# Kernel optimization log

Hardware: AMD Instinct MI355X
Metric: run time of the kernel (lower is better)

Reference implementation:

```python
import jax, jax.numpy as jnp
import numpy as np

B, T, H = 16, 2048, 768
HH = H // 2          # LSTM hidden per direction
L = 2                # interaction layers
NH = 8               # attention heads
SA, SO = 24, 24      # num aspect / opinion spans
WMAX = 16            # max span width (static)


def _make_spans(key, n_spans):
    # non-overlapping spans: one per chunk of size T//n_spans, width in [1, WMAX]
    chunk = T // n_spans
    k1, k2 = jax.random.split(key)
    off = jax.random.randint(k1, (B, n_spans), 0, chunk - WMAX)
    width = jax.random.randint(k2, (B, n_spans), 1, WMAX + 1)
    starts = jnp.arange(n_spans, dtype=jnp.int32)[None, :] * chunk + off
    return jnp.stack([starts, starts + width], axis=-1).astype(jnp.int32)


def setup_inputs() -> dict:
    key = jax.random.key(0)
    ks = jax.random.split(key, 20)
    p = lambda k, shape: jax.random.normal(k, shape, jnp.float32) * 0.02
    inp = {
        'hidden_states': jax.random.normal(ks[0], (B, T, H), jnp.float32),
        'aspect_spans': _make_spans(ks[1], SA),
        'opinion_spans': _make_spans(ks[2], SO),
    }
    # bidirectional LSTM span encoders (gate order i,f,g,o; bias = b_ih + b_hh)
    ki = 3
    for pre in ('a', 'o'):
        for d in ('f', 'b'):
            inp[f'{pre}_wih_{d}'] = p(ks[ki], (4 * HH, H)); ki += 1
            inp[f'{pre}_whh_{d}'] = p(ks[ki], (4 * HH, HH)); ki += 1
            inp[f'{pre}_b_{d}'] = jnp.zeros((4 * HH,), jnp.float32)
    # cross-attention stacks (torch nn.MultiheadAttention layout)
    for pre in ('ao', 'oa'):
        inp[f'attn_{pre}_in_w'] = p(ks[ki], (L, 3 * H, H)); ki += 1
        inp[f'attn_{pre}_in_b'] = jnp.zeros((L, 3 * H), jnp.float32)
        inp[f'attn_{pre}_out_w'] = p(ks[ki], (L, H, H)); ki += 1
        inp[f'attn_{pre}_out_b'] = jnp.zeros((L, H), jnp.float32)
    inp['ln_a_g'] = jnp.ones((L, H), jnp.float32)
    inp['ln_a_b'] = jnp.zeros((L, H), jnp.float32)
    inp['ln_o_g'] = jnp.ones((L, H), jnp.float32)
    inp['ln_o_b'] = jnp.zeros((L, H), jnp.float32)
    # span_interaction_projection: Linear(2H,H) -> ReLU -> Linear(H,H); stored [in,out]
    inp['p_w1'] = p(ks[ki], (2 * H, H)); ki += 1
    inp['p_b1'] = jnp.zeros((H,), jnp.float32)
    inp['p_w2'] = p(ks[ki], (H, H)); ki += 1
    inp['p_b2'] = jnp.zeros((H,), jnp.float32)
    return inp


def _lstm_span_encode(hs, spans, wih_f, whh_f, b_f, wih_b, whh_b, b_b):
    # batched replacement for the per-span python-loop LSTM calls
    Bn, Tn, Hd = hs.shape
    S = spans.shape[1]
    starts = jnp.clip(spans[..., 0], 0, Tn - 1)
    ends = jnp.clip(spans[..., 1], starts + 1, Tn)
    lens = (ends - starts).reshape(Bn * S)                              # [N]
    idx = jnp.clip(starts[..., None] + jnp.arange(WMAX), 0, Tn - 1)     # [B,S,W]
    x = hs[jnp.arange(Bn)[:, None, None], idx].reshape(Bn * S, WMAX, Hd)
    mask = jnp.arange(WMAX)[None, :] < lens[:, None]                    # [N,W]

    def step(carry, inp):
        h, c = carry
        x_t, m = inp
        g = x_t @ wih_f.T + h @ whh_f.T + b_f
        i, f, gg, o = jnp.split(g, 4, axis=-1)
        c_new = jax.nn.sigmoid(f) * c + jax.nn.sigmoid(i) * jnp.tanh(gg)
        h_new = jax.nn.sigmoid(o) * jnp.tanh(c_new)
        m = m[:, None]
        return (jnp.where(m, h_new, h), jnp.where(m, c_new, c)), None

    N = Bn * S
    h0 = jnp.zeros((N, HH), hs.dtype)
    (h_fwd, _), _ = jax.lax.scan(step, (h0, h0), (jnp.swapaxes(x, 0, 1), mask.T))
    # backward direction output at the original last step == one cell step from zero state
    x_last = jnp.take_along_axis(x, (lens - 1)[:, None, None], axis=1)[:, 0, :]
    g = x_last @ wih_b.T + b_b
    i, f, gg, o = jnp.split(g, 4, axis=-1)
    c_b = jax.nn.sigmoid(i) * jnp.tanh(gg)
    h_bwd = jax.nn.sigmoid(o) * jnp.tanh(c_b)
    return jnp.concatenate([h_fwd, h_bwd], -1).reshape(Bn, S, 2 * HH)


def _mha(q, kv, in_w, in_b, out_w, out_b):
    E = q.shape[-1]
    hd = E // NH
    wq, wk, wv = jnp.split(in_w, 3, axis=0)
    bq, bk, bv = jnp.split(in_b, 3, axis=0)
    qh = (q @ wq.T + bq).reshape(q.shape[0], q.shape[1], NH, hd)
    kh = (kv @ wk.T + bk).reshape(kv.shape[0], kv.shape[1], NH, hd)
    vh = (kv @ wv.T + bv).reshape(kv.shape[0], kv.shape[1], NH, hd)
    att = jax.nn.softmax(jnp.einsum('bqhd,bkhd->bhqk', qh, kh) * (1.0 / np.sqrt(hd)), axis=-1)
    out = jnp.einsum('bhqk,bkhd->bqhd', att, vh).reshape(q.shape)
    return out @ out_w.T + out_b


def _ln(x, g, b):
    mu = x.mean(-1, keepdims=True)
    var = ((x - mu) ** 2).mean(-1, keepdims=True)
    return (x - mu) * jax.lax.rsqrt(var + 1e-5) * g + b


def _apply_spans(tok, spans, reps, p_w1, p_b1, p_w2, p_b2):
    # vectorized version of the per-token projection loop (spans non-overlapping per set)
    Bn, Tn, Hd = tok.shape
    t = jnp.arange(Tn)
    starts = spans[..., 0]
    ends = jnp.minimum(spans[..., 1], Tn)
    cov = (t[None, :, None] >= starts[:, None, :]) & (t[None, :, None] < ends[:, None, :])  # [B,T,S]
    covered = cov.any(-1)
    sidx = jnp.argmax(cov, -1)                                   # [B,T]
    rep = reps[jnp.arange(Bn)[:, None], sidx]                    # [B,T,H]
    h1 = jax.nn.relu(jnp.concatenate([tok, rep], -1) @ p_w1 + p_b1)
    new = h1 @ p_w2 + p_b2
    return jnp.where(covered[..., None], new, tok)


def reference(hidden_states, a_wih_f, a_whh_f, a_b_f, a_wih_b, a_whh_b, a_b_b,
              o_wih_f, o_whh_f, o_b_f, o_wih_b, o_whh_b, o_b_b,
              attn_ao_in_w, attn_ao_in_b, attn_ao_out_w, attn_ao_out_b,
              attn_oa_in_w, attn_oa_in_b, attn_oa_out_w, attn_oa_out_b,
              ln_a_g, ln_a_b, ln_o_g, ln_o_b,
              p_w1, p_b1, p_w2, p_b2,
              aspect_spans, opinion_spans):
    ea = _lstm_span_encode(hidden_states, aspect_spans, a_wih_f, a_whh_f, a_b_f, a_wih_b, a_whh_b, a_b_b)
    eo = _lstm_span_encode(hidden_states, opinion_spans, o_wih_f, o_whh_f, o_b_f, o_wih_b, o_whh_b, o_b_b)
    for l in range(L):
        ea = _ln(ea + _mha(ea, eo, attn_ao_in_w[l], attn_ao_in_b[l], attn_ao_out_w[l], attn_ao_out_b[l]),
                 ln_a_g[l], ln_a_b[l])
        eo = _ln(eo + _mha(eo, ea, attn_oa_in_w[l], attn_oa_in_b[l], attn_oa_out_w[l], attn_oa_out_b[l]),
                 ln_o_g[l], ln_o_b[l])
    tok = _apply_spans(hidden_states, aspect_spans, ea, p_w1, p_b1, p_w2, p_b2)
    tok = _apply_spans(tok, opinion_spans, eo, p_w1, p_b1, p_w2, p_b2)
    return tok
```

## Files before the change

### kernel.cpp

```cpp
#include <hip/hip_runtime.h>
#include <cstddef>
#include <cstdint>

#define DI __device__ __forceinline__

namespace {

typedef short short8 __attribute__((ext_vector_type(8)));
typedef float f32x4 __attribute__((ext_vector_type(4)));

constexpr int B_ = 16, T_ = 2048, H_ = 768, HH_ = 384, NSPAN_ = 24;
constexpr int NS_ = B_ * NSPAN_;
constexpr int G4_ = 4 * HH_;
constexpr int WMAX_ = 16;
constexpr int MAXTOK_ = NS_ * WMAX_;

constexpr size_t W_AWIF = 0;
constexpr size_t W_OWIF = 1179648;
constexpr size_t W_AWIB = 2359296;
constexpr size_t W_OWIB = 3538944;
constexpr size_t W_AWHH = 4718592;
constexpr size_t W_OWHH = 5308416;
constexpr size_t W_AOIN = 5898240;
constexpr size_t W_OAIN = 9437184;
constexpr size_t W_AOOUT = 12976128;
constexpr size_t W_OAOUT = 14155776;
constexpr size_t W_PW1T = 15335424;
constexpr size_t W_PW2T = 16515072;
constexpr size_t W_TOTEL = 17104896;

constexpr size_t WB_B   = 0;
constexpr size_t WB_SZ  = W_TOTEL * 2;
constexpr size_t XGSZ_B = (size_t)NS_ * 16 * G4_ * 2;
constexpr size_t XGA_B  = WB_B + WB_SZ;
constexpr size_t XGO_B  = XGA_B + XGSZ_B;
constexpr size_t QKV_B  = XGO_B + XGSZ_B;
constexpr size_t AOT_B  = QKV_B + (size_t)NS_ * 2304 * 4;
constexpr size_t RT_B   = AOT_B + (size_t)NS_ * H_ * 4;
constexpr size_t EA_B   = RT_B + (size_t)NS_ * H_ * 4;
constexpr size_t EO_B   = EA_B + (size_t)NS_ * H_ * 4;
constexpr size_t HB_B   = EO_B + (size_t)NS_ * H_ * 4;
constexpr size_t CST_B  = HB_B + 2ull * 2 * 384 * 384 * 2;
constexpr size_t INT_B  = CST_B + 2ull * 384 * 384 * 4;
constexpr size_t I_STARTS = 0;
constexpr size_t I_LENS   = I_STARTS + 2 * NS_;
constexpr size_t I_ORD    = I_LENS + 2 * NS_;
constexpr size_t I_SLENS  = I_ORD + 2 * NS_;
constexpr size_t I_XGLIST = I_SLENS + 2 * NS_;
constexpr size_t I_TOKLIST = I_XGLIST + 2 * MAXTOK_;
constexpr size_t I_CNT    = I_TOKLIST + 2 * MAXTOK_;

DI float sigf(float x) { return 1.f / (1.f + __expf(-x)); }
DI float tanhfast(float x) {
  x = fminf(fmaxf(x, -15.f), 15.f);
  float e = __expf(2.f * x);
  return (e - 1.f) / (e + 1.f);
}
DI unsigned short f2bf(float f) {
  unsigned u = __float_as_uint(f);
  return (unsigned short)((u + 0x7fffu + ((u >> 16) & 1u)) >> 16);
}
DI unsigned pk2(float lo, float hi) {
  return (unsigned)f2bf(lo) | ((unsigned)f2bf(hi) << 16);
}
DI float bf2f(unsigned short u) { return __uint_as_float(((unsigned)u) << 16); }

struct PJ { const float* src; unsigned short* dst; int n; int R; int C; int tr; };
struct PREP { PJ j[12]; };

__global__ __launch_bounds__(256) void prep_w(PREP pp) {
  PJ job = pp.j[blockIdx.y];
  int stride = gridDim.x * blockDim.x;
  int g = blockIdx.x * blockDim.x + threadIdx.x;
  if (!job.tr) {
    int n4 = job.n >> 2;
    for (int i = g; i < n4; i += stride) {
      float4 v = ((const float4*)job.src)[i];
      ushort4 o;
      o.x = f2bf(v.x); o.y = f2bf(v.y); o.z = f2bf(v.z); o.w = f2bf(v.w);
      ((ushort4*)job.dst)[i] = o;
    }
  } else {
    for (int i = g; i < job.n; i += stride) {
      int r = i / job.C, c = i - r * job.C;
      job.dst[(size_t)c * job.R + r] = f2bf(job.src[i]);
    }
  }
}

__global__ void span_meta(const int* __restrict__ asp, const int* __restrict__ osp,
                          int* __restrict__ starts, int* __restrict__ lens,
                          int* __restrict__ xglist, int* __restrict__ cnt) {
  int i = blockIdx.x * blockDim.x + threadIdx.x;
  if (i >= 2 * NS_) return;
  int type = i / NS_, sp = i - type * NS_;
  const int* spans = type ? osp : asp;
  int s0 = spans[2 * sp], s1 = spans[2 * sp + 1];
  int st = min(max(s0, 0), T_ - 1);
  int en = min(max(s1, st + 1), T_);
  int ln = min(en - st, WMAX_);
  starts[i] = st;
  lens[i] = ln;
  for (int t = 0; t < ln; ++t) {
    int pos = atomicAdd(&cnt[type], 1);
    if (pos < MAXTOK_) xglist[type * MAXTOK_ + pos] = (sp << 4) | t;
  }
}

__global__ void sort_spans(const int* __restrict__ lens, int* __restrict__ ord,
                           int* __restrict__ slens) {
  int type = blockIdx.x;
  __shared__ int ls[NS_];
  __shared__ int os[NS_];
  __shared__ int hist[WMAX_], off[WMAX_];
  int tid = threadIdx.x;
  if (tid < WMAX_) hist[tid] = 0;
  __syncthreads();
  int myl = 1;
  if (tid < NS_) {
    myl = lens[type * NS_ + tid];
    ls[tid] = myl;
    atomicAdd(&hist[WMAX_ - myl], 1);
  }
  __syncthreads();
  if (tid == 0) { int a = 0; for (int b = 0; b < WMAX_; ++b) { off[b] = a; a += hist[b]; } }
  __syncthreads();
  if (tid < NS_) { int pos = atomicAdd(&off[WMAX_ - myl], 1); os[pos] = tid; }
  __syncthreads();
  if (tid < NS_) { int sp = os[tid]; ord[type * NS_ + tid] = sp; slens[type * NS_ + tid] = ls[sp]; }
}

__global__ void cov_build(const int* __restrict__ asp, const int* __restrict__ osp,
                          int* __restrict__ toklist, int* __restrict__ cnt2) {
  int i = blockIdx.x * blockDim.x + threadIdx.x;
  if (i >= 2 * NS_) return;
  int type = i / NS_, sp = i - type * NS_;
  const int* spans = type ? osp : asp;
  int b = sp / NSPAN_, s = sp - b * NSPAN_;
  int s0 = spans[2 * sp];
  int s1 = min(spans[2 * sp + 1], T_);
  int lo = max(s0, 0), hi = min(s1, s0 + WMAX_);
  for (int tt = lo; tt < hi; ++tt) {
    int pos = atomicAdd(&cnt2[type], 1);
    if (pos < MAXTOK_) toklist[type * MAXTOK_ + pos] = (b * T_ + tt) | (s << 20);
  }
}

enum { M_XG = 0, M_XGB = 1, M_QKV = 2, M_OUTP = 3, M_AP1 = 4, M_AP2 = 5 };

struct GP {
  const float* A;
  const float* A2;
  const unsigned short* Wb;
  const unsigned short* Ab;
  const float* bias;
  const float* resid;
  float* C;
  unsigned short* Cb;
  const int* list;
  const int* cnt;
  const int* starts;
  const int* lens;
  int K;
};

template <int MODE>
__global__ __launch_bounds__(256) void mgemm(GP p) {
  __shared__ __align__(16) unsigned short As[128 * 64];
  __shared__ __align__(16) unsigned short Bs[128 * 64];
  const int tid = threadIdx.x;
  const int m0 = blockIdx.x * 128, n0 = blockIdx.y * 128;
  int rows = NS_;
  if constexpr (MODE == M_XG || MODE == M_AP1 || MODE == M_AP2) rows = min(*p.cnt, MAXTOK_);
  if (m0 >= rows) return;

  const int ar = tid >> 1, kh = tid & 1;
  const int lr = m0 + ar;
  const bool aok = lr < rows;
  const float* aptr = nullptr;
  const float* aptr2 = nullptr;
  const unsigned short* abptr = nullptr;
  if (aok) {
    if constexpr (MODE == M_XG) {
      int e = p.list[lr]; int sp = e >> 4, tt = e & 15;
      int srow = min(p.starts[sp] + tt, T_ - 1);
      aptr = p.A + ((size_t)((sp / NSPAN_) * T_ + srow)) * H_;
    } else if constexpr (MODE == M_XGB) {
      int sp = lr;
      int srow = min(max(p.starts[sp] + p.lens[sp] - 1, 0), T_ - 1);
      aptr = p.A + ((size_t)((sp / NSPAN_) * T_ + srow)) * H_;
    } else if constexpr (MODE == M_QKV) {
      aptr = ((n0 < H_) ? p.A : p.A2) + (size_t)lr * H_;
    } else if constexpr (MODE == M_OUTP) {
      aptr = p.A + (size_t)lr * H_;
    } else if constexpr (MODE == M_AP1) {
      int e = p.list[lr]; int bt = e & 0xFFFFF; int s = e >> 20;
      aptr = p.A + (size_t)bt * H_;
      aptr2 = p.A2 + ((size_t)((bt >> 11) * NSPAN_ + s)) * H_;
    } else {
      abptr = p.Ab + (size_t)lr * H_;
    }
  }
  const unsigned short* brow = p.Wb + (size_t)(n0 + ar) * p.K;

  const int lane = tid & 63, wv = tid >> 6, wr = wv >> 1, wc = wv & 1;
  const int abase_r = wr * 64 + (lane & 15);
  const int bbase_r = wc * 64 + (lane & 15);
  const int kcol = lane >> 4;
  const int swz = (lane & 7) << 4;

  f32x4 acc[4][4];
#pragma unroll
  for (int mi = 0; mi < 4; ++mi)
#pragma unroll
    for (int ni = 0; ni < 4; ++ni) acc[mi][ni] = (f32x4){0.f, 0.f, 0.f, 0.f};

  for (int k0 = 0; k0 < p.K; k0 += 64) {
    if constexpr (MODE == M_AP2) {
      if (aok) {
        const unsigned short* s = abptr + k0 + kh * 32;
#pragma unroll
        for (int c = 0; c < 4; ++c)
          *(uint4*)((char*)As + ar * 128 + ((((kh * 4 + c) * 16)) ^ ((ar & 7) << 4))) =
              *(const uint4*)(s + c * 8);
      }
    } else {
      if (aok) {
#pragma unroll
        for (int c = 0; c < 4; ++c) {
          int kg = k0 + kh * 32 + c * 8;
          const float* s;
          if constexpr (MODE == M_AP1) s = (kg < H_) ? (aptr + kg) : (aptr2 + (kg - H_));
          else s = aptr + kg;
          float4 u = *(const float4*)s;
          float4 v = *(const float4*)(s + 4);
          uint4 w;
          w.x = pk2(u.x, u.y); w.y = pk2(u.z, u.w);
          w.z = pk2(v.x, v.y); w.w = pk2(v.z, v.w);
          *(uint4*)((char*)As + ar * 128 + ((((kh * 4 + c) * 16)) ^ ((ar & 7) << 4))) = w;
        }
      }
    }
    {
      const unsigned short* s = brow + k0 + kh * 32;
#pragma unroll
      for (int c = 0; c < 4; ++c)
        *(uint4*)((char*)Bs + ar * 128 + ((((kh * 4 + c) * 16)) ^ ((ar & 7) << 4))) =
            *(const uint4*)(s + c * 8);
    }
    __syncthreads();
#pragma unroll
    for (int ks = 0; ks < 2; ++ks) {
      short8 af[4], bq[4];
#pragma unroll
      for (int i = 0; i < 4; ++i)
        af[i] = *(const short8*)((char*)As + (abase_r + i * 16) * 128 +
                                 (((ks * 4 + kcol) * 16) ^ swz));
#pragma unroll
      for (int i = 0; i < 4; ++i)
        bq[i] = *(const short8*)((char*)Bs + (bbase_r + i * 16) * 128 +
                                 (((ks * 4 + kcol) * 16) ^ swz));
#pragma unroll
      for (int mi = 0; mi < 4; ++mi)
#pragma unroll
        for (int ni = 0; ni < 4; ++ni)
          acc[mi][ni] = __builtin_amdgcn_mfma_f32_16x16x32_bf16(af[mi], bq[ni], acc[mi][ni], 0, 0, 0);
    }
    __syncthreads();
  }

#pragma unroll
  for (int mi = 0; mi < 4; ++mi) {
#pragma unroll
    for (int q = 0; q < 4; ++q) {
      int row = m0 + wr * 64 + mi * 16 + (lane >> 4) * 4 + q;
      if (row >= rows) continue;
      if constexpr (MODE == M_XG) {
        int e = p.list[row]; int sp = e >> 4, tt = e & 15;
        unsigned short* cr = p.Cb + ((size_t)(sp * 16 + tt)) * G4_;
#pragma unroll
        for (int ni = 0; ni < 4; ++ni) {
          int col = n0 + wc * 64 + ni * 16 + (lane & 15);
          cr[col] = f2bf(acc[mi][ni][q] + p.bias[col]);
        }
      } else if constexpr (MODE == M_XGB) {
        float* cr = p.C + (size_t)row * G4_;
#pragma unroll
        for (int ni = 0; ni < 4; ++ni) {
          int col = n0 + wc * 64 + ni * 16 + (lane & 15);
          cr[col] = acc[mi][ni][q] + p.bias[col];
        }
      } else if constexpr (MODE == M_QKV) {
        float* cr = p.C + (size_t)row * 2304;
#pragma unroll
        for (int ni = 0; ni < 4; ++ni) {
          int col = n0 + wc * 64 + ni * 16 + (lane & 15);
          cr[col] = acc[mi][ni][q] + p.bias[col];
        }
      } else if constexpr (MODE == M_OUTP) {
        float* cr = p.C + (size_t)row * H_;
#pragma unroll
        for (int ni = 0; ni < 4; ++ni) {
          int col = n0 + wc * 64 + ni * 16 + (lane & 15);
          cr[col] = acc[mi][ni][q] + p.bias[col] + p.resid[(size_t)row * H_ + col];
        }
      } else if constexpr (MODE == M_AP1) {
        unsigned short* cr = p.Cb + (size_t)row * H_;
#pragma unroll
        for (int ni = 0; ni < 4; ++ni) {
          int col = n0 + wc * 64 + ni * 16 + (lane & 15);
          cr[col] = f2bf(fmaxf(acc[mi][ni][q] + p.bias[col], 0.f));
        }
      } else {
        int e = p.list[row]; int bt = e & 0xFFFFF;
        float* cr = p.C + (size_t)bt * H_;
#pragma unroll
        for (int ni = 0; ni < 4; ++ni) {
          int col = n0 + wc * 64 + ni * 16 + (lane & 15);
          cr[col] = acc[mi][ni][q] + p.bias[col];
        }
      }
    }
  }
}

__global__ void bwd_act(const float* __restrict__ gb, float* __restrict__ ea,
                        float* __restrict__ eo) {
  int idx = blockIdx.x * 256 + threadIdx.x;
  if (idx >= 2 * NS_ * HH_) return;
  int type = idx / (NS_ * HH_);
  int rem = idx - type * NS_ * HH_;
  int sp = rem / HH_, j = rem - sp * HH_;
  const float* g = gb + ((size_t)type * NS_ + sp) * G4_;
  float cb = sigf(g[j]) * tanhfast(g[2 * HH_ + j]);
  float hb = sigf(g[3 * HH_ + j]) * tanhfast(cb);
  (type ? eo : ea)[(size_t)sp * H_ + HH_ + j] = hb;
}

struct LP {
  const unsigned short* hr;
  unsigned short* hw;
  float* c;
  const unsigned short* xg_a;
  const unsigned short* xg_o;
  const unsigned short* whh_a;
  const unsigned short* whh_o;
  const int* ord; const int* slens;
  int t;
};

__global__ __launch_bounds__(256) void lstm_mfma(LP p) {
  const int type = blockIdx.z;
  const int m0 = blockIdx.x * 128;
  const int jb = blockIdx.y * 32;
  const int tid = threadIdx.x;
  const unsigned short* hr = p.hr + (size_t)type * 384 * 384;
  unsigned short* hw = p.hw + (size_t)type * 384 * 384;
  const int* slens = p.slens + type * NS_;

  if (slens[m0] <= p.t) {
    int r = tid >> 1, ch = tid & 1;
    const unsigned short* s = hr + (size_t)(m0 + r) * 384 + jb + ch * 16;
    unsigned short* d = hw + (size_t)(m0 + r) * 384 + jb + ch * 16;
    *(uint4*)d = *(const uint4*)s;
    *(uint4*)(d + 8) = *(const uint4*)(s + 8);
    return;
  }

  const unsigned short* xg = type ? p.xg_o : p.xg_a;
  const unsigned short* whh = type ? p.whh_o : p.whh_a;
  const int* ordt = p.ord + type * NS_;
  float* cst = p.c + (size_t)type * 384 * 384;

  __shared__ __align__(16) unsigned short As[128 * 64];
  __shared__ __align__(16) unsigned short Bs[128 * 64];

  const int ar = tid >> 1, kh = tid & 1;
  const unsigned short* arow = hr + (size_t)(m0 + ar) * 384;
  const int ng = ((ar >> 4) & 3) * HH_ + jb + (ar >> 6) * 16 + (ar & 15);
  const unsigned short* brow = whh + (size_t)ng * HH_;

  const int lane = tid & 63, wv = tid >> 6, wr = wv >> 1, wc = wv & 1;
  const int abase_r = wr * 64 + (lane & 15);
  const int bbase_r = wc * 64 + (lane & 15);
  const int kcol = lane >> 4;
  const int swz = (lane & 7) << 4;

  f32x4 acc[4][4];
#pragma unroll
  for (int mi = 0; mi < 4; ++mi)
#pragma unroll
    for (int ni = 0; ni < 4; ++ni) acc[mi][ni] = (f32x4){0.f, 0.f, 0.f, 0.f};

  for (int k0 = 0; k0 < HH_; k0 += 64) {
    const unsigned short* sa = arow + k0 + kh * 32;
    const unsigned short* sb = brow + k0 + kh * 32;
#pragma unroll
    for (int c = 0; c < 4; ++c) {
      *(uint4*)((char*)As + ar * 128 + ((((kh * 4 + c) * 16)) ^ ((ar & 7) << 4))) =
          *(const uint4*)(sa + c * 8);
      *(uint4*)((char*)Bs + ar * 128 + ((((kh * 4 + c) * 16)) ^ ((ar & 7) << 4))) =
          *(const uint4*)(sb + c * 8);
    }
    __syncthreads();
#pragma unroll
    for (int ks = 0; ks < 2; ++ks) {
      short8 af[4], bq[4];
#pragma unroll
      for (int i = 0; i < 4; ++i)
        af[i] = *(const short8*)((char*)As + (abase_r + i * 16) * 128 +
                                 (((ks * 4 + kcol) * 16) ^ swz));
#pragma unroll
      for (int i = 0; i < 4; ++i)
        bq[i] = *(const short8*)((char*)Bs + (bbase_r + i * 16) * 128 +
                                 (((ks * 4 + kcol) * 16) ^ swz));
#pragma unroll
      for (int mi = 0; mi < 4; ++mi)
#pragma unroll
        for (int ni = 0; ni < 4; ++ni)
          acc[mi][ni] = __builtin_amdgcn_mfma_f32_16x16x32_bf16(af[mi], bq[ni], acc[mi][ni], 0, 0, 0);
    }
    __syncthreads();
  }

  const int col = jb + wc * 16 + (lane & 15);
#pragma unroll
  for (int mi = 0; mi < 4; ++mi) {
#pragma unroll
    for (int q = 0; q < 4; ++q) {
      int row = m0 + wr * 64 + mi * 16 + (lane >> 4) * 4 + q;
      int sp = ordt[row];
      bool act = p.t < slens[row];
      const unsigned short* xr = xg + ((size_t)(sp * 16 + p.t)) * G4_;
      float gi = acc[mi][0][q] + bf2f(xr[col]);
      float gf = acc[mi][1][q] + bf2f(xr[HH_ + col]);
      float gg = acc[mi][2][q] + bf2f(xr[2 * HH_ + col]);
      float go = acc[mi][3][q] + bf2f(xr[3 * HH_ + col]);
      size_t hidx = (size_t)row * 384 + col;
      unsigned short hraw = hr[hidx];
      float co = cst[hidx];
      float cn = sigf(gf) * co + sigf(gi) * tanhfast(gg);
      float hn = sigf(go) * tanhfast(cn);
      hw[hidx] = act ? f2bf(hn) : hraw;
      if (act) cst[hidx] = cn;
    }
  }
}

__global__ void finalize_h(const unsigned short* __restrict__ hfin,
                           const int* __restrict__ ord,
                           float* __restrict__ ea, float* __restrict__ eo) {
  int idx = blockIdx.x * 256 + threadIdx.x;
  if (idx >= 2 * 384 * 384) return;
  int type = idx / (384 * 384);
  int rem = idx - type * 384 * 384;
  int srt = rem / 384, j = rem - srt * 384;
  int sp = ord[type * NS_ + srt];
  (type ? eo : ea)[(size_t)sp * H_ + j] =
      bf2f(hfin[(size_t)type * 384 * 384 + (size_t)srt * 384 + j]);
}

__global__ __launch_bounds__(256) void attn_core(const float* __restrict__ qkv,
                                                 float* __restrict__ aot) {
  int b = blockIdx.x >> 3, h = blockIdx.x & 7;
  __shared__ float qs[24][97], ks[24][97], vs[24][97];
  __shared__ float sc[24][25];
  __shared__ float sinv[24];
  int tid = threadIdx.x;
  for (int idx = tid; idx < 24 * 96; idx += 256) {
    int s = idx / 96, d = idx - s * 96;
    size_t rb = ((size_t)(b * 24 + s)) * 2304 + h * 96 + d;
    qs[s][d] = qkv[rb];
    ks[s][d] = qkv[rb + H_];
    vs[s][d] = qkv[rb + 2 * H_];
  }
  __syncthreads();
  for (int pp = tid; pp < 576; pp += 256) {
    int qi = pp / 24, ki = pp - qi * 24;
    float a = 0.f;
    for (int d = 0; d < 96; ++d) a = fmaf(qs[qi][d], ks[ki][d], a);
    sc[qi][ki] = a * 0.10206207261596577f;
  }
  __syncthreads();
  if (tid < 24) {
    float m = -1e30f;
    for (int k2 = 0; k2 < 24; ++k2) m = fmaxf(m, sc[tid][k2]);
    float ssum = 0.f;
    for (int k2 = 0; k2 < 24; ++k2) { float e = __expf(sc[tid][k2] - m); sc[tid][k2] = e; ssum += e; }
    sinv[tid] = 1.f / ssum;
  }
  __syncthreads();
  for (int idx = tid; idx < 24 * 96; idx += 256) {
    int s = idx / 96, d = idx - s * 96;
    float a = 0.f;
    for (int k2 = 0; k2 < 24; ++k2) a = fmaf(sc[s][k2], vs[k2][d], a);
    aot[((size_t)(b * 24 + s)) * H_ + h * 96 + d] = a * sinv[s];
  }
}

__global__ __launch_bounds__(256) void ln_k(const float* __restrict__ x,
                                            const float* __restrict__ g,
                                            const float* __restrict__ bb,
                                            float* __restrict__ dst) {
  int row = blockIdx.x;
  const float* xr = x + (size_t)row * H_;
  float vals[3];
  float s1 = 0.f, s2 = 0.f;
#pragma unroll
  for (int u = 0; u < 3; ++u) {
    float v = xr[threadIdx.x + 256 * u];
    vals[u] = v; s1 += v; s2 += v * v;
  }
  for (int o = 32; o > 0; o >>= 1) { s1 += __shfl_down(s1, o, 64); s2 += __shfl_down(s2, o, 64); }
  __shared__ float r1[4], r2[4];
  __shared__ float mu_s, rs_s;
  int w = threadIdx.x >> 6, lane = threadIdx.x & 63;
  if (lane == 0) { r1[w] = s1; r2[w] = s2; }
  __syncthreads();
  if (threadIdx.x == 0) {
    float t1 = r1[0] + r1[1] + r1[2] + r1[3];
    float t2 = r2[0] + r2[1] + r2[2] + r2[3];
    float mu = t1 / (float)H_;
    float var = t2 / (float)H_ - mu * mu;
    mu_s = mu; rs_s = rsqrtf(var + 1e-5f);
  }
  __syncthreads();
#pragma unroll
  for (int u = 0; u < 3; ++u) {
    int c = threadIdx.x + 256 * u;
    dst[(size_t)row * H_ + c] = (vals[u] - mu_s) * rs_s * g[c] + bb[c];
  }
}

}

extern "C" void kernel_launch(void* const* d_in, const int* in_sizes, int n_in,
                              void* d_out, int out_size, void* d_ws, size_t ws_size,
                              hipStream_t stream) {
  (void)in_sizes; (void)n_in; (void)out_size; (void)ws_size;
  const float* hs = (const float*)d_in[0];
  const int* asp = (const int*)d_in[1];
  const int* osp = (const int*)d_in[2];
  const float* a_wih_f = (const float*)d_in[3];
  const float* a_whh_f = (const float*)d_in[4];
  const float* a_b_f   = (const float*)d_in[5];
  const float* a_wih_b = (const float*)d_in[6];
  const float* a_b_b   = (const float*)d_in[8];
  const float* o_wih_f = (const float*)d_in[9];
  const float* o_whh_f = (const float*)d_in[10];
  const float* o_b_f   = (const float*)d_in[11];
  const float* o_wih_b = (const float*)d_in[12];
  const float* o_b_b   = (const float*)d_in[14];
  const float* ao_in_w  = (const float*)d_in[15];
  const float* ao_in_b  = (const float*)d_in[16];
  const float* ao_out_w = (const float*)d_in[17];
  const float* ao_out_b = (const float*)d_in[18];
  const float* oa_in_w  = (const float*)d_in[19];
  const float* oa_in_b  = (const float*)d_in[20];
  const float* oa_out_w = (const float*)d_in[21];
  const float* oa_out_b = (const float*)d_in[22];
  const float* ln_a_g = (const float*)d_in[23];
  const float* ln_a_b = (const float*)d_in[24];
  const float* ln_o_g = (const float*)d_in[25];
  const float* ln_o_b = (const float*)d_in[26];
  const float* p_w1 = (const float*)d_in[27];
  const float* p_b1 = (const float*)d_in[28];
  const float* p_w2 = (const float*)d_in[29];
  const float* p_b2 = (const float*)d_in[30];
  float* out = (float*)d_out;

  char* ws = (char*)d_ws;
  unsigned short* WB = (unsigned short*)(ws + WB_B);
  unsigned short* xga = (unsigned short*)(ws + XGA_B);
  unsigned short* xgo = (unsigned short*)(ws + XGO_B);
  float* qkv = (float*)(ws + QKV_B);
  float* aot = (float*)(ws + AOT_B);
  float* rt  = (float*)(ws + RT_B);
  float* ea  = (float*)(ws + EA_B);
  float* eo  = (float*)(ws + EO_B);
  unsigned short* hb = (unsigned short*)(ws + HB_B);
  float* cst = (float*)(ws + CST_B);
  float* gb  = (float*)(ws + QKV_B);
  unsigned short* h1b = (unsigned short*)(ws + XGA_B);
  int* I = (int*)(ws + INT_B);
  int* starts = I + I_STARTS;
  int* lens   = I + I_LENS;
  int* ord    = I + I_ORD;
  int* slens  = I + I_SLENS;
  int* xglist = I + I_XGLIST;
  int* toklist = I + I_TOKLIST;
  int* cnt    = I + I_CNT;

  hipMemcpyAsync(out, hs, (size_t)B_ * T_ * H_ * sizeof(float),
                 hipMemcpyDeviceToDevice, stream);
  hipMemsetAsync(cnt, 0, 4 * sizeof(int), stream);
  hipMemsetAsync(ws + HB_B, 0, (CST_B - HB_B) + 2ull * 384 * 384 * 4, stream);

  {
    PREP pp;
    pp.j[0]  = {a_wih_f,  WB + W_AWIF,  1536 * 768, 0, 0, 0};
    pp.j[1]  = {o_wih_f,  WB + W_OWIF,  1536 * 768, 0, 0, 0};
    pp.j[2]  = {a_wih_b,  WB + W_AWIB,  1536 * 768, 0, 0, 0};
    pp.j[3]  = {o_wih_b,  WB + W_OWIB,  1536 * 768, 0, 0, 0};
    pp.j[4]  = {a_whh_f,  WB + W_AWHH,  1536 * 384, 0, 0, 0};
    pp.j[5]  = {o_whh_f,  WB + W_OWHH,  1536 * 384, 0, 0, 0};
    pp.j[6]  = {ao_in_w,  WB + W_AOIN,  2 * 2304 * 768, 0, 0, 0};
    pp.j[7]  = {oa_in_w,  WB + W_OAIN,  2 * 2304 * 768, 0, 0, 0};
    pp.j[8]  = {ao_out_w, WB + W_AOOUT, 2 * 768 * 768, 0, 0, 0};
    pp.j[9]  = {oa_out_w, WB + W_OAOUT, 2 * 768 * 768, 0, 0, 0};
    pp.j[10] = {p_w1,     WB + W_PW1T,  1536 * 768, 1536, 768, 1};
    pp.j[11] = {p_w2,     WB + W_PW2T,  768 * 768,  768,  768, 1};
    prep_w<<<dim3(512, 12), 256, 0, stream>>>(pp);
  }

  span_meta<<<3, 256, 0, stream>>>(asp, osp, starts, lens, xglist, cnt);
  sort_spans<<<2, 384, 0, stream>>>(lens, ord, slens);
  cov_build<<<3, 256, 0, stream>>>(asp, osp, toklist, cnt + 2);

  {
    GP g{}; g.A = hs; g.Wb = WB + W_AWIF; g.bias = a_b_f; g.Cb = xga;
    g.list = xglist; g.cnt = cnt; g.starts = starts; g.K = H_;
    mgemm<M_XG><<<dim3(48, 12), 256, 0, stream>>>(g);
  }
  {
    GP g{}; g.A = hs; g.Wb = WB + W_OWIF; g.bias = o_b_f; g.Cb = xgo;
    g.list = xglist + MAXTOK_; g.cnt = cnt + 1; g.starts = starts + NS_; g.K = H_;
    mgemm<M_XG><<<dim3(48, 12), 256, 0, stream>>>(g);
  }
  {
    GP g{}; g.A = hs; g.Wb = WB + W_AWIB; g.bias = a_b_b; g.C = gb;
    g.starts = starts; g.lens = lens; g.K = H_;
    mgemm<M_XGB><<<dim3(3, 12), 256, 0, stream>>>(g);
  }
  {
    GP g{}; g.A = hs; g.Wb = WB + W_OWIB; g.bias = o_b_b; g.C = gb + (size_t)NS_ * G4_;
    g.starts = starts + NS_; g.lens = lens + NS_; g.K = H_;
    mgemm<M_XGB><<<dim3(3, 12), 256, 0, stream>>>(g);
  }
  bwd_act<<<(2 * NS_ * HH_ + 255) / 256, 256, 0, stream>>>(gb, ea, eo);

  for (int t = 0; t < 16; ++t) {
    LP lp{};
    lp.hr = hb + (size_t)(t & 1) * 2 * 384 * 384;
    lp.hw = hb + (size_t)((t + 1) & 1) * 2 * 384 * 384;
    lp.c = cst;
    lp.xg_a = xga; lp.xg_o = xgo;
    lp.whh_a = WB + W_AWHH; lp.whh_o = WB + W_OWHH;
    lp.ord = ord; lp.slens = slens; lp.t = t;
    lstm_mfma<<<dim3(3, 12, 2), 256, 0, stream>>>(lp);
  }
  finalize_h<<<(2 * 384 * 384 + 255) / 256, 256, 0, stream>>>(hb, ord, ea, eo);

  for (int l = 0; l < 2; ++l) {
    for (int dir = 0; dir < 2; ++dir) {
      float* q  = dir ? eo : ea;
      float* kv = dir ? ea : eo;
      const unsigned short* inw = WB + (dir ? W_OAIN : W_AOIN) + (size_t)l * 2304 * 768;
      const float* inb = (dir ? oa_in_b : ao_in_b) + (size_t)l * 3 * H_;
      const unsigned short* ow = WB + (dir ? W_OAOUT : W_AOOUT) + (size_t)l * 768 * 768;
      const float* ob = (dir ? oa_out_b : ao_out_b) + (size_t)l * H_;
      const float* lg = (dir ? ln_o_g : ln_a_g) + (size_t)l * H_;
      const float* lb = (dir ? ln_o_b : ln_a_b) + (size_t)l * H_;
      {
        GP g{}; g.A = q; g.A2 = kv; g.Wb = inw; g.bias = inb; g.C = qkv; g.K = H_;
        mgemm<M_QKV><<<dim3(3, 18), 256, 0, stream>>>(g);
      }
      attn_core<<<128, 256, 0, stream>>>(qkv, aot);
      {
        GP g{}; g.A = aot; g.Wb = ow; g.bias = ob; g.resid = q; g.C = rt; g.K = H_;
        mgemm<M_OUTP><<<dim3(3, 6), 256, 0, stream>>>(g);
      }
      ln_k<<<NS_, 256, 0, stream>>>(rt, lg, lb, q);
    }
  }

  for (int type = 0; type < 2; ++type) {
    {
      GP g{}; g.A = out; g.A2 = type ? eo : ea; g.Wb = WB + W_PW1T; g.bias = p_b1; g.Cb = h1b;
      g.list = toklist + (size_t)type * MAXTOK_; g.cnt = cnt + 2 + type; g.K = 2 * H_;
      mgemm<M_AP1><<<dim3(48, 6), 256, 0, stream>>>(g);
    }
    {
      GP g{}; g.Ab = h1b; g.Wb = WB + W_PW2T; g.bias = p_b2; g.C = out;
      g.list = toklist + (size_t)type * MAXTOK_; g.cnt = cnt + 2 + type; g.K = H_;
      mgemm<M_AP2><<<dim3(48, 6), 256, 0, stream>>>(g);
    }
  }
}
```

Before: 1.519 ms.

## Fuse span metadata kernels, fuse backward LSTM gates, tile weight transpose

Merges span_meta, sort_spans and cov_build into one block-wide scan kernel, which replaces global atomics with deterministic prefix sums and drops the counter memset. Fuses the backward-direction input GEMMs for both span types with the gate activation into a single MFMA kernel whose weight rows are permuted so the i/g/o gates land in the same lanes, removing the intermediate gate buffer. The transposing weight conversion now goes through a shared-memory tile so global accesses are coalesced. The LSTM step also skips the h-buffer copy when a span finished more than one step earlier, relying on double-buffer parity.

```diff
diff --git a/kernel.cpp b/kernel.cpp
--- a/kernel.cpp
+++ b/kernel.cpp
@@ -70,9 +70,9 @@
 
 __global__ __launch_bounds__(256) void prep_w(PREP pp) {
   PJ job = pp.j[blockIdx.y];
-  int stride = gridDim.x * blockDim.x;
-  int g = blockIdx.x * blockDim.x + threadIdx.x;
   if (!job.tr) {
+    int stride = gridDim.x * blockDim.x;
+    int g = blockIdx.x * blockDim.x + threadIdx.x;
     int n4 = job.n >> 2;
     for (int i = g; i < n4; i += stride) {
       float4 v = ((const float4*)job.src)[i];
@@ -81,72 +81,99 @@
       ((ushort4*)job.dst)[i] = o;
     }
   } else {
-    for (int i = g; i < job.n; i += stride) {
-      int r = i / job.C, c = i - r * job.C;
-      job.dst[(size_t)c * job.R + r] = f2bf(job.src[i]);
-    }
-  }
-}
-
-__global__ void span_meta(const int* __restrict__ asp, const int* __restrict__ osp,
-                          int* __restrict__ starts, int* __restrict__ lens,
-                          int* __restrict__ xglist, int* __restrict__ cnt) {
-  int i = blockIdx.x * blockDim.x + threadIdx.x;
-  if (i >= 2 * NS_) return;
-  int type = i / NS_, sp = i - type * NS_;
+    __shared__ unsigned short tile[32][34];
+    int R = job.R, C = job.C;
+    int tcn = C >> 5, trn = R >> 5;
+    int tx = threadIdx.x & 31, ty = threadIdx.x >> 5;
+    for (int tid2 = blockIdx.x; tid2 < trn * tcn; tid2 += gridDim.x) {
+      int trr = (tid2 / tcn) << 5, tcc = (tid2 % tcn) << 5;
+      __syncthreads();
+#pragma unroll
+      for (int k = 0; k < 4; ++k)
+        tile[ty + 8 * k][tx] = f2bf(job.src[(size_t)(trr + ty + 8 * k) * C + tcc + tx]);
+      __syncthreads();
+#pragma unroll
+      for (int k = 0; k < 4; ++k)
+        job.dst[(size_t)(tcc + ty + 8 * k) * R + trr + tx] = tile[tx][ty + 8 * k];
+    }
+  }
+}
+
+__global__ __launch_bounds__(768) void span_prep(
+    const int* __restrict__ asp, const int* __restrict__ osp,
+    int* __restrict__ starts, int* __restrict__ lens,
+    int* __restrict__ ord, int* __restrict__ slens,
+    int* __restrict__ xglist, int* __restrict__ toklist, int* __restrict__ cnt) {
+  int tid = threadIdx.x;
+  int type = tid / NS_, sp = tid - type * NS_;
   const int* spans = type ? osp : asp;
   int s0 = spans[2 * sp], s1 = spans[2 * sp + 1];
   int st = min(max(s0, 0), T_ - 1);
   int en = min(max(s1, st + 1), T_);
   int ln = min(en - st, WMAX_);
-  starts[i] = st;
-  lens[i] = ln;
-  for (int t = 0; t < ln; ++t) {
-    int pos = atomicAdd(&cnt[type], 1);
-    if (pos < MAXTOK_) xglist[type * MAXTOK_ + pos] = (sp << 4) | t;
-  }
-}
-
-__global__ void sort_spans(const int* __restrict__ lens, int* __restrict__ ord,
-                           int* __restrict__ slens) {
-  int type = blockIdx.x;
-  __shared__ int ls[NS_];
-  __shared__ int os[NS_];
-  __shared__ int hist[WMAX_], off[WMAX_];
-  int tid = threadIdx.x;
-  if (tid < WMAX_) hist[tid] = 0;
-  __syncthreads();
-  int myl = 1;
-  if (tid < NS_) {
-    myl = lens[type * NS_ + tid];
-    ls[tid] = myl;
-    atomicAdd(&hist[WMAX_ - myl], 1);
-  }
-  __syncthreads();
-  if (tid == 0) { int a = 0; for (int b = 0; b < WMAX_; ++b) { off[b] = a; a += hist[b]; } }
-  __syncthreads();
-  if (tid < NS_) { int pos = atomicAdd(&off[WMAX_ - myl], 1); os[pos] = tid; }
-  __syncthreads();
-  if (tid < NS_) { int sp = os[tid]; ord[type * NS_ + tid] = sp; slens[type * NS_ + tid] = ls[sp]; }
-}
-
-__global__ void cov_build(const int* __restrict__ asp, const int* __restrict__ osp,
-                          int* __restrict__ toklist, int* __restrict__ cnt2) {
-  int i = blockIdx.x * blockDim.x + threadIdx.x;
-  if (i >= 2 * NS_) return;
-  int type = i / NS_, sp = i - type * NS_;
-  const int* spans = type ? osp : asp;
-  int b = sp / NSPAN_, s = sp - b * NSPAN_;
-  int s0 = spans[2 * sp];
-  int s1 = min(spans[2 * sp + 1], T_);
-  int lo = max(s0, 0), hi = min(s1, s0 + WMAX_);
-  for (int tt = lo; tt < hi; ++tt) {
-    int pos = atomicAdd(&cnt2[type], 1);
-    if (pos < MAXTOK_) toklist[type * MAXTOK_ + pos] = (b * T_ + tt) | (s << 20);
-  }
-}
-
-enum { M_XG = 0, M_XGB = 1, M_QKV = 2, M_OUTP = 3, M_AP1 = 4, M_AP2 = 5 };
+  starts[tid] = st;
+  lens[tid] = ln;
+  int clo = max(s0, 0), chi = min(s1, T_);
+  int cln = max(chi - clo, 0);
+
+  __shared__ int sx[768];
+  __shared__ int t0s, t0c;
+  sx[tid] = ln;
+  __syncthreads();
+  for (int off = 1; off < 768; off <<= 1) {
+    int v = (tid >= off) ? sx[tid - off] : 0;
+    __syncthreads();
+    sx[tid] += v;
+    __syncthreads();
+  }
+  if (tid == NS_ - 1) t0s = sx[tid];
+  __syncthreads();
+  {
+    int base = sx[tid] - ln - (type ? t0s : 0);
+    for (int t = 0; t < ln; ++t) {
+      int pos = base + t;
+      if (pos < MAXTOK_) xglist[type * MAXTOK_ + pos] = (sp << 4) | t;
+    }
+    if (tid == NS_ - 1) cnt[0] = sx[tid];
+    if (tid == 767) cnt[1] = sx[767] - t0s;
+  }
+  __syncthreads();
+  sx[tid] = cln;
+  __syncthreads();
+  for (int off = 1; off < 768; off <<= 1) {
+    int v = (tid >= off) ? sx[tid - off] : 0;
+    __syncthreads();
+    sx[tid] += v;
+    __syncthreads();
+  }
+  if (tid == NS_ - 1) t0c = sx[tid];
+  __syncthreads();
+  {
+    int base = sx[tid] - cln - (type ? t0c : 0);
+    int b = sp / NSPAN_, slocal = sp - b * NSPAN_;
+    for (int t = 0; t < cln; ++t) {
+      int pos = base + t;
+      if (pos < MAXTOK_) toklist[type * MAXTOK_ + pos] = (b * T_ + clo + t) | (slocal << 20);
+    }
+    if (tid == NS_ - 1) cnt[2] = sx[tid];
+    if (tid == 767) cnt[3] = sx[767] - t0c;
+  }
+  __shared__ int hist[2][WMAX_], hoff[2][WMAX_];
+  if (tid < 2 * WMAX_) hist[tid / WMAX_][tid % WMAX_] = 0;
+  __syncthreads();
+  atomicAdd(&hist[type][WMAX_ - ln], 1);
+  __syncthreads();
+  if (tid < 2) {
+    int a = 0;
+    for (int bkt = 0; bkt < WMAX_; ++bkt) { hoff[tid][bkt] = a; a += hist[tid][bkt]; }
+  }
+  __syncthreads();
+  int pos = atomicAdd(&hoff[type][WMAX_ - ln], 1);
+  ord[type * NS_ + pos] = sp;
+  slens[type * NS_ + pos] = ln;
+}
+
+enum { M_XG = 0, M_QKV = 2, M_OUTP = 3, M_AP1 = 4, M_AP2 = 5 };
 
 struct GP {
   const float* A;
@@ -160,7 +187,6 @@
   const int* list;
   const int* cnt;
   const int* starts;
-  const int* lens;
   int K;
 };
 
@@ -184,10 +210,6 @@
     if constexpr (MODE == M_XG) {
       int e = p.list[lr]; int sp = e >> 4, tt = e & 15;
       int srow = min(p.starts[sp] + tt, T_ - 1);
-      aptr = p.A + ((size_t)((sp / NSPAN_) * T_ + srow)) * H_;
-    } else if constexpr (MODE == M_XGB) {
-      int sp = lr;
-      int srow = min(max(p.starts[sp] + p.lens[sp] - 1, 0), T_ - 1);
       aptr = p.A + ((size_t)((sp / NSPAN_) * T_ + srow)) * H_;
     } else if constexpr (MODE == M_QKV) {
       aptr = ((n0 < H_) ? p.A : p.A2) + (size_t)lr * H_;
@@ -283,13 +305,6 @@
           int col = n0 + wc * 64 + ni * 16 + (lane & 15);
           cr[col] = f2bf(acc[mi][ni][q] + p.bias[col]);
         }
-      } else if constexpr (MODE == M_XGB) {
-        float* cr = p.C + (size_t)row * G4_;
-#pragma unroll
-        for (int ni = 0; ni < 4; ++ni) {
-          int col = n0 + wc * 64 + ni * 16 + (lane & 15);
-          cr[col] = acc[mi][ni][q] + p.bias[col];
-        }
       } else if constexpr (MODE == M_QKV) {
         float* cr = p.C + (size_t)row * 2304;
 #pragma unroll
@@ -324,17 +339,94 @@
   }
 }
 
-__global__ void bwd_act(const float* __restrict__ gb, float* __restrict__ ea,
-                        float* __restrict__ eo) {
-  int idx = blockIdx.x * 256 + threadIdx.x;
-  if (idx >= 2 * NS_ * HH_) return;
-  int type = idx / (NS_ * HH_);
-  int rem = idx - type * NS_ * HH_;
-  int sp = rem / HH_, j = rem - sp * HH_;
-  const float* g = gb + ((size_t)type * NS_ + sp) * G4_;
-  float cb = sigf(g[j]) * tanhfast(g[2 * HH_ + j]);
-  float hb = sigf(g[3 * HH_ + j]) * tanhfast(cb);
-  (type ? eo : ea)[(size_t)sp * H_ + HH_ + j] = hb;
+struct XBP {
+  const float* hs;
+  const unsigned short* wa; const unsigned short* wo;
+  const float* ba; const float* bo;
+  float* ea; float* eo;
+  const int* starts; const int* lens;
+};
+
+__global__ __launch_bounds__(256) void xgb_mfma(XBP p) {
+  const int type = blockIdx.z;
+  const int m0 = blockIdx.x * 128, jb = blockIdx.y * 32;
+  const int tid = threadIdx.x;
+  const unsigned short* wb = type ? p.wo : p.wa;
+  const float* bias = type ? p.bo : p.ba;
+  const int* starts = p.starts + type * NS_;
+  const int* lens = p.lens + type * NS_;
+  float* dst = type ? p.eo : p.ea;
+
+  __shared__ __align__(16) unsigned short As[128 * 64];
+  __shared__ __align__(16) unsigned short Bs[128 * 64];
+
+  const int ar = tid >> 1, kh = tid & 1;
+  const int spA = m0 + ar;
+  int srow = min(max(starts[spA] + lens[spA] - 1, 0), T_ - 1);
+  const float* aptr = p.hs + ((size_t)((spA / NSPAN_) * T_ + srow)) * H_;
+  const int ng = ((ar >> 4) & 3) * HH_ + jb + (ar >> 6) * 16 + (ar & 15);
+  const unsigned short* brow = wb + (size_t)ng * H_;
+
+  const int lane = tid & 63, wv = tid >> 6, wr = wv >> 1, wc = wv & 1;
+  const int abase_r = wr * 64 + (lane & 15);
+  const int bbase_r = wc * 64 + (lane & 15);
+  const int kcol = lane >> 4;
+  const int swz = (lane & 7) << 4;
+
+  f32x4 acc[4][4];
+#pragma unroll
+  for (int mi = 0; mi < 4; ++mi)
+#pragma unroll
+    for (int ni = 0; ni < 4; ++ni) acc[mi][ni] = (f32x4){0.f, 0.f, 0.f, 0.f};
+
+  for (int k0 = 0; k0 < H_; k0 += 64) {
+#pragma unroll
+    for (int c = 0; c < 4; ++c) {
+      const float* s = aptr + k0 + kh * 32 + c * 8;
+      float4 u = *(const float4*)s;
+      float4 v = *(const float4*)(s + 4);
+      uint4 w;
+      w.x = pk2(u.x, u.y); w.y = pk2(u.z, u.w);
+      w.z = pk2(v.x, v.y); w.w = pk2(v.z, v.w);
+      *(uint4*)((char*)As + ar * 128 + ((((kh * 4 + c) * 16)) ^ ((ar & 7) << 4))) = w;
+      *(uint4*)((char*)Bs + ar * 128 + ((((kh * 4 + c) * 16)) ^ ((ar & 7) << 4))) =
+          *(const uint4*)(brow + k0 + kh * 32 + c * 8);
+    }
+    __syncthreads();
+#pragma unroll
+    for (int ks = 0; ks < 2; ++ks) {
+      short8 af[4], bq[4];
+#pragma unroll
+      for (int i = 0; i < 4; ++i)
+        af[i] = *(const short8*)((char*)As + (abase_r + i * 16) * 128 +
+                                 (((ks * 4 + kcol) * 16) ^ swz));
+#pragma unroll
+      for (int i = 0; i < 4; ++i)
+        bq[i] = *(const short8*)((char*)Bs + (bbase_r + i * 16) * 128 +
+                                 (((ks * 4 + kcol) * 16) ^ swz));
+#pragma unroll
+      for (int mi = 0; mi < 4; ++mi)
+#pragma unroll
+        for (int ni = 0; ni < 4; ++ni)
+          acc[mi][ni] = __builtin_amdgcn_mfma_f32_16x16x32_bf16(af[mi], bq[ni], acc[mi][ni], 0, 0, 0);
+    }
+    __syncthreads();
+  }
+
+  const int col = jb + wc * 16 + (lane & 15);
+#pragma unroll
+  for (int mi = 0; mi < 4; ++mi) {
+#pragma unroll
+    for (int q = 0; q < 4; ++q) {
+      int row = m0 + wr * 64 + mi * 16 + (lane >> 4) * 4 + q;
+      float gi = acc[mi][0][q] + bias[col];
+      float gg = acc[mi][2][q] + bias[2 * HH_ + col];
+      float go = acc[mi][3][q] + bias[3 * HH_ + col];
+      float cb = sigf(gi) * tanhfast(gg);
+      float hb = sigf(go) * tanhfast(cb);
+      dst[(size_t)row * H_ + HH_ + col] = hb;
+    }
+  }
 }
 
 struct LP {
@@ -358,12 +450,15 @@
   unsigned short* hw = p.hw + (size_t)type * 384 * 384;
   const int* slens = p.slens + type * NS_;
 
-  if (slens[m0] <= p.t) {
-    int r = tid >> 1, ch = tid & 1;
-    const unsigned short* s = hr + (size_t)(m0 + r) * 384 + jb + ch * 16;
-    unsigned short* d = hw + (size_t)(m0 + r) * 384 + jb + ch * 16;
-    *(uint4*)d = *(const uint4*)s;
-    *(uint4*)(d + 8) = *(const uint4*)(s + 8);
+  int maxlen = slens[m0];
+  if (maxlen <= p.t) {
+    if (maxlen == p.t) {
+      int r = tid >> 1, ch = tid & 1;
+      const unsigned short* s = hr + (size_t)(m0 + r) * 384 + jb + ch * 16;
+      unsigned short* d = hw + (size_t)(m0 + r) * 384 + jb + ch * 16;
+      *(uint4*)d = *(const uint4*)s;
+      *(uint4*)(d + 8) = *(const uint4*)(s + 8);
+    }
     return;
   }
 
@@ -580,7 +675,6 @@
   float* eo  = (float*)(ws + EO_B);
   unsigned short* hb = (unsigned short*)(ws + HB_B);
   float* cst = (float*)(ws + CST_B);
-  float* gb  = (float*)(ws + QKV_B);
   unsigned short* h1b = (unsigned short*)(ws + XGA_B);
   int* I = (int*)(ws + INT_B);
   int* starts = I + I_STARTS;
@@ -593,7 +687,6 @@
 
   hipMemcpyAsync(out, hs, (size_t)B_ * T_ * H_ * sizeof(float),
                  hipMemcpyDeviceToDevice, stream);
-  hipMemsetAsync(cnt, 0, 4 * sizeof(int), stream);
   hipMemsetAsync(ws + HB_B, 0, (CST_B - HB_B) + 2ull * 384 * 384 * 4, stream);
 
   {
@@ -613,9 +706,8 @@
     prep_w<<<dim3(512, 12), 256, 0, stream>>>(pp);
   }
 
-  span_meta<<<3, 256, 0, stream>>>(asp, osp, starts, lens, xglist, cnt);
-  sort_spans<<<2, 384, 0, stream>>>(lens, ord, slens);
-  cov_build<<<3, 256, 0, stream>>>(asp, osp, toklist, cnt + 2);
+  span_prep<<<1, 768, 0, stream>>>(asp, osp, starts, lens, ord, slens,
+                                   xglist, toklist, cnt);
 
   {
     GP g{}; g.A = hs; g.Wb = WB + W_AWIF; g.bias = a_b_f; g.Cb = xga;
@@ -628,16 +720,12 @@
     mgemm<M_XG><<<dim3(48, 12), 256, 0, stream>>>(g);
   }
   {
-    GP g{}; g.A = hs; g.Wb = WB + W_AWIB; g.bias = a_b_b; g.C = gb;
-    g.starts = starts; g.lens = lens; g.K = H_;
-    mgemm<M_XGB><<<dim3(3, 12), 256, 0, stream>>>(g);
-  }
-  {
-    GP g{}; g.A = hs; g.Wb = WB + W_OWIB; g.bias = o_b_b; g.C = gb + (size_t)NS_ * G4_;
-    g.starts = starts + NS_; g.lens = lens + NS_; g.K = H_;
-    mgemm<M_XGB><<<dim3(3, 12), 256, 0, stream>>>(g);
-  }
-  bwd_act<<<(2 * NS_ * HH_ + 255) / 256, 256, 0, stream>>>(gb, ea, eo);
+    XBP x{};
+    x.hs = hs; x.wa = WB + W_AWIB; x.wo = WB + W_OWIB;
+    x.ba = a_b_b; x.bo = o_b_b; x.ea = ea; x.eo = eo;
+    x.starts = starts; x.lens = lens;
+    xgb_mfma<<<dim3(3, 12, 2), 256, 0, stream>>>(x);
+  }
 
   for (int t = 0; t < 16; ++t) {
     LP lp{};
```

After: 1.283 ms. 15.5% less time.
